# Kernel optimization log

Measured on AMD Instinct MI355X. Metric: run time of the kernel, lower is better.

The kernel has to match this reference:

```python
import jax, jax.numpy as jnp
import numpy as np

DIM = 384
RES = 32
NH = 8
RD = 2
B = 64


def _linear_params(key, out_f, in_f, scale=0.02, bias=True):
    kw, kb = jax.random.split(key)
    W = jax.random.normal(kw, (out_f, in_f), dtype=jnp.float32) * scale
    b = jax.random.normal(kb, (out_f,), dtype=jnp.float32) * scale if bias else None
    return W, b


def setup_inputs() -> dict:
    key = jax.random.key(0)
    ks = jax.random.split(key, 16)
    x = jax.random.normal(ks[0], (B, RES, RES, DIM), dtype=jnp.float32)
    Wc_h, bc_h = _linear_params(ks[1], NH * RD, DIM)
    Wg_h, bg_h = _linear_params(ks[2], RES * RES, RES * RD)
    Wo_h, bo_h = _linear_params(ks[3], DIM, DIM)
    Wc_w, bc_w = _linear_params(ks[4], NH * RD, DIM)
    Wg_w, bg_w = _linear_params(ks[5], RES * RES, RES * RD)
    Wo_w, bo_w = _linear_params(ks[6], DIM, DIM)
    Wmlpc, _ = _linear_params(ks[7], DIM, DIM, bias=False)
    Wr1, br1 = _linear_params(ks[8], DIM // 4, DIM)
    Wr2, br2 = _linear_params(ks[9], DIM * 3, DIM // 4)
    Wp, bp = _linear_params(ks[10], DIM, DIM)
    return dict(x=x, Wc_h=Wc_h, bc_h=bc_h, Wg_h=Wg_h, bg_h=bg_h, Wo_h=Wo_h, bo_h=bo_h,
                Wc_w=Wc_w, bc_w=bc_w, Wg_w=Wg_w, bg_w=bg_w, Wo_w=Wo_w, bo_w=bo_w,
                Wmlpc=Wmlpc, Wr1=Wr1, br1=br1, Wr2=Wr2, br2=br2, Wp=Wp, bp=bp)


def _dynamixer_op(x, Wc, bc, Wg, bg, Wo, bo):
    # x: [N, L, C]
    N, L, C = x.shape
    hd = C // NH
    # compress -> [N, L, NH*RD] -> [N, NH, L*RD]
    w = x @ Wc.T + bc
    w = w.reshape(N, L, NH, RD).transpose(0, 2, 1, 3).reshape(N, NH, L * RD)
    # generate -> [N, NH, L, L], softmax over axis -2 (rows)
    w = (w @ Wg.T + bg).reshape(N, NH, L, L)
    w = jax.nn.softmax(w, axis=-2)
    # x -> [N, NH, hd, L]; mix: y[n,h,d,j] = sum_l x[n,h,d,l] * w[n,h,l,j]
    xh = x.reshape(N, L, NH, hd).transpose(0, 2, 3, 1)
    y = jnp.einsum('nhdl,nhlj->nhdj', xh, w)
    y = y.transpose(0, 3, 1, 2).reshape(N, L, C)
    return y @ Wo.T + bo


def reference(x, Wc_h, bc_h, Wg_h, bg_h, Wo_h, bo_h,
              Wc_w, bc_w, Wg_w, bg_w, Wo_w, bo_w,
              Wmlpc, Wr1, br1, Wr2, br2, Wp, bp):
    Bn, H, W, C = x.shape
    # mix along H: batch over (B, W)
    h = _dynamixer_op(x.transpose(0, 2, 1, 3).reshape(Bn * W, H, C),
                      Wc_h, bc_h, Wg_h, bg_h, Wo_h, bo_h)
    h = h.reshape(Bn, W, H, C).transpose(0, 2, 1, 3)
    # mix along W: batch over (B, H)
    w = _dynamixer_op(x.reshape(Bn * H, W, C),
                      Wc_w, bc_w, Wg_w, bg_w, Wo_w, bo_w)
    w = w.reshape(Bn, H, W, C)
    # channel path (no bias)
    c = x @ Wmlpc.T
    # reweighting: global average pool over H, W
    a = (h + w + c).mean(axis=(1, 2))            # [B, C]
    a = jax.nn.gelu(a @ Wr1.T + br1, approximate=False) @ Wr2.T + br2  # [B, 3C]
    a = a.reshape(Bn, C, 3).transpose(2, 0, 1)   # [3, B, C]
    a = jax.nn.softmax(a, axis=0)[:, :, None, None, :]  # [3, B, 1, 1, C]
    out = h * a[0] + w * a[1] + c * a[2]
    return out @ Wp.T + bp
```

## Files before the change

kernel.cpp:

```cpp
#include <hip/hip_runtime.h>

typedef unsigned short u16;
typedef __bf16 bf16_t;
typedef bf16_t bf16x8 __attribute__((ext_vector_type(8)));
typedef float f32x4 __attribute__((ext_vector_type(4)));

__device__ __forceinline__ u16 f2b(float f) {
  union { float f; unsigned u; } v; v.f = f;
  unsigned r = (v.u + 0x7fffu + ((v.u >> 16) & 1u)) >> 16;
  return (u16)r;
}
__device__ __forceinline__ float b2f(u16 b) {
  union { unsigned u; float f; } v; v.u = ((unsigned)b) << 16;
  return v.f;
}
__device__ __forceinline__ f32x4 mfma16(bf16x8 a, bf16x8 b, f32x4 c) {
  return __builtin_amdgcn_mfma_f32_16x16x32_bf16(a, b, c, 0, 0, 0);
}

struct CvtJobs {
  const float* s[8];
  u16* d[8];
  int n[8];
};
__global__ void k0_cvt(CvtJobs j) {
  int job = blockIdx.y;
  const float* s = j.s[job];
  u16* d = j.d[job];
  int n = j.n[job];
  int stride = gridDim.x * blockDim.x * 4;
  for (int i = (blockIdx.x * blockDim.x + threadIdx.x) * 4; i < n; i += stride) {
    float4 v = *(const float4*)(s + i);
    ushort4 o4;
    o4.x = f2b(v.x); o4.y = f2b(v.y); o4.z = f2b(v.z); o4.w = f2b(v.w);
    *(ushort4*)(d + i) = o4;
  }
}

#define LW 392
#define TW 40
#define AW 40

__global__ __launch_bounds__(256, 2) void k1_mixer(
    const float* __restrict__ x,
    const u16* __restrict__ Wc_h_b, const float* __restrict__ bc_h,
    const u16* __restrict__ Wg_h_b, const float* __restrict__ bg_h,
    const u16* __restrict__ Wc_w_b, const float* __restrict__ bc_w,
    const u16* __restrict__ Wg_w_b, const float* __restrict__ bg_w,
    u16* __restrict__ y_h, u16* y_w,
    float* __restrict__ psum_yh, float* __restrict__ psum_yw,
    float* __restrict__ psum_x)
{
  __shared__ u16 xs_b[32 * LW];
  __shared__ u16 xs_t[384 * TW];
  __shared__ u16 attn[8 * 32 * AW];
  __shared__ u16 whead[16 * 72];

  const int tid = threadIdx.x;
  const int bid = blockIdx.x;
  const int path = bid >> 11;
  const int n = bid & 2047;
  const int b = n >> 5, o = n & 31;
  long base; int strideL;
  if (path == 0) { base = (long)b * 393216 + (long)o * 384;   strideL = 12288; }
  else           { base = (long)b * 393216 + (long)o * 12288; strideL = 384; }
  const float* xseq = x + base;

  const u16* Wc_b = path ? Wc_w_b : Wc_h_b;
  const float* bc = path ? bc_w : bc_h;
  const u16* Wg_b = path ? Wg_w_b : Wg_h_b;
  const float* bg = path ? bg_w : bg_h;

  for (int i = tid; i < 3072; i += 256) {
    int l = i / 96, c4 = (i % 96) * 4;
    float4 v = *(const float4*)(xseq + (long)l * strideL + c4);
    ushort4 w4;
    w4.x = f2b(v.x); w4.y = f2b(v.y); w4.z = f2b(v.z); w4.w = f2b(v.w);
    *(ushort4*)&xs_b[l * LW + c4] = w4;
  }
  for (int i = tid; i < 576; i += 256) whead[576 + i] = 0;
  __syncthreads();

  for (int i = tid; i < 3072; i += 256) {
    int c = i % 384, l4 = (i / 384) * 4;
    ushort4 w4;
    w4.x = xs_b[(l4 + 0) * LW + c];
    w4.y = xs_b[(l4 + 1) * LW + c];
    w4.z = xs_b[(l4 + 2) * LW + c];
    w4.w = xs_b[(l4 + 3) * LW + c];
    *(ushort4*)&xs_t[c * TW + l4] = w4;
  }
  if (path == 0) {
    for (int c = tid; c < 384; c += 256) {
      float s = 0.f;
      for (int l = 0; l < 32; l++) s += b2f(xs_b[l * LW + c]);
      psum_x[(long)n * 384 + c] = s;
    }
  }

  const int wave = tid >> 6, lane = tid & 63;
  const int lq = lane >> 4, lr = lane & 15;
  const f32x4 z = {0.f, 0.f, 0.f, 0.f};

  if (wave < 2) {
    f32x4 acc = z;
    for (int ks = 0; ks < 12; ks++) {
      bf16x8 af  = *(const bf16x8*)&xs_b[(wave * 16 + lr) * LW + ks * 32 + lq * 8];
      bf16x8 bfr = *(const bf16x8*)(Wc_b + lr * 384 + ks * 32 + lq * 8);
      acc = mfma16(af, bfr, acc);
    }
    float bcv = bc[lr];
    for (int r = 0; r < 4; r++) {
      int l = wave * 16 + lq * 4 + r;
      whead[(lr >> 1) * 72 + l * 2 + (lr & 1)] = f2b(acc[r] + bcv);
    }
  }
  __syncthreads();

  {
    bf16x8 ga0 = *(const bf16x8*)&whead[lr * 72 + lq * 8];
    bf16x8 ga1 = *(const bf16x8*)&whead[lr * 72 + 32 + lq * 8];
    for (int t = 0; t < 16; t++) {
      int nt = wave * 16 + t;
      const u16* wg = Wg_b + (nt * 16 + lr) * 64;
      bf16x8 gb0 = *(const bf16x8*)(wg + lq * 8);
      bf16x8 gb1 = *(const bf16x8*)(wg + 32 + lq * 8);
      f32x4 acc = z;
      acc = mfma16(ga0, gb0, acc);
      acc = mfma16(ga1, gb1, acc);
      if (lq < 2) {
        int m = nt * 16 + lr, ii = m >> 5, jj = m & 31;
        for (int r = 0; r < 4; r++)
          attn[((lq * 4 + r) * 32 + jj) * AW + ii] = f2b(acc[r]);
      }
    }
  }
  __syncthreads();

  {
    int h = tid >> 5, j = tid & 31;
    u16* row = &attn[(h * 32 + j) * AW];
    float v[32]; float mx = -1e30f;
    for (int i = 0; i < 32; i++) {
      v[i] = b2f(row[i]) + bg[i * 32 + j];
      mx = fmaxf(mx, v[i]);
    }
    float s = 0.f;
    for (int i = 0; i < 32; i++) { v[i] = __expf(v[i] - mx); s += v[i]; }
    float inv = 1.0f / s;
    for (int i = 0; i < 32; i++) row[i] = f2b(v[i] * inv);
  }
  __syncthreads();

  for (int hh = 0; hh < 2; hh++) {
    int h = wave * 2 + hh;
    bf16x8 bf0 = *(const bf16x8*)&attn[(h * 32 + lr) * AW + lq * 8];
    bf16x8 bf1 = *(const bf16x8*)&attn[(h * 32 + 16 + lr) * AW + lq * 8];
    for (int mt = 0; mt < 3; mt++) {
      bf16x8 af = *(const bf16x8*)&xs_t[(h * 48 + mt * 16 + lr) * TW + lq * 8];
      f32x4 a0 = mfma16(af, bf0, z);
      f32x4 a1 = mfma16(af, bf1, z);
      for (int r = 0; r < 4; r++) {
        int c = h * 48 + mt * 16 + lq * 4 + r;
        xs_b[lr * LW + c]        = f2b(a0[r]);
        xs_b[(16 + lr) * LW + c] = f2b(a1[r]);
      }
    }
  }
  __syncthreads();

  if (path == 0) {
    u16* yout = y_h + base;
    for (int i = tid; i < 1536; i += 256) {
      int l = i / 48, uu = (i % 48) * 8;
      *(uint4*)(yout + (long)l * 12288 + uu) = *(const uint4*)&xs_b[l * LW + uu];
    }
  } else {
    u16* yout = y_w + (long)(n * 32) * 768;
    for (int i = tid; i < 1536; i += 256) {
      int l = i / 48, uu = (i % 48) * 8;
      *(uint4*)(yout + (long)l * 768 + uu) = *(const uint4*)&xs_b[l * LW + uu];
    }
  }
  {
    float* pdst = (path ? psum_yw : psum_yh) + (long)n * 384;
    for (int c = tid; c < 384; c += 256) {
      float s = 0.f;
      for (int jj = 0; jj < 32; jj++) s += b2f(xs_b[jj * LW + c]);
      pdst[c] = s;
    }
  }
}

__global__ __launch_bounds__(384) void k3_scales(
    const float* __restrict__ psum_yh, const float* __restrict__ psum_yw,
    const float* __restrict__ psum_x,
    const float* __restrict__ Wo_h, const float* __restrict__ bo_h,
    const float* __restrict__ Wo_w, const float* __restrict__ bo_w,
    const float* __restrict__ Wmlpc,
    const float* __restrict__ Wr1, const float* __restrict__ br1,
    const float* __restrict__ Wr2, const float* __restrict__ br2,
    float* __restrict__ scal)
{
  __shared__ float ph[384], pw[384], px[384], a[384], r1[96];
  int b = blockIdx.x, t = threadIdx.x;
  float sh = 0.f, sw = 0.f, sx = 0.f;
  for (int o = 0; o < 32; o++) {
    sh += psum_yh[(long)(b * 32 + o) * 384 + t];
    sw += psum_yw[(long)(b * 32 + o) * 384 + t];
    sx += psum_x[(long)(b * 32 + o) * 384 + t];
  }
  ph[t] = sh; pw[t] = sw; px[t] = sx;
  __syncthreads();
  float s1 = 0.f, s2 = 0.f, s3 = 0.f;
  for (int k = 0; k < 384; k++) {
    s1 += ph[k] * Wo_h[t * 384 + k];
    s2 += pw[k] * Wo_w[t * 384 + k];
    s3 += px[k] * Wmlpc[t * 384 + k];
  }
  a[t] = (s1 + s2 + s3) * (1.f / 1024.f) + bo_h[t] + bo_w[t];
  __syncthreads();
  if (t < 96) {
    float s = 0.f;
    for (int k = 0; k < 384; k++) s += a[k] * Wr1[t * 384 + k];
    s += br1[t];
    r1[t] = s * 0.5f * (1.f + erff(s * 0.70710678118654752f));
  }
  __syncthreads();
  {
    float sv[3];
    for (int si = 0; si < 3; si++) {
      float acc = 0.f;
      for (int k = 0; k < 96; k++) acc += r1[k] * Wr2[(t * 3 + si) * 96 + k];
      sv[si] = acc + br2[t * 3 + si];
    }
    float mx = fmaxf(sv[0], fmaxf(sv[1], sv[2]));
    float e0 = __expf(sv[0] - mx), e1 = __expf(sv[1] - mx), e2 = __expf(sv[2] - mx);
    float inv = 1.f / (e0 + e1 + e2);
    scal[0 * 24576 + b * 384 + t] = e0 * inv;
    scal[1 * 24576 + b * 384 + t] = e1 * inv;
    scal[2 * 24576 + b * 384 + t] = e2 * inv;
  }
}

__device__ __forceinline__ void gemm_regB(
    const u16* __restrict__ Bglob, const u16* __restrict__ bufA,
    f32x4 acc[4][3], int wn, int lq, int lr)
{
  const u16* bp0 = Bglob + (wn * 48 + lr) * 384 + lq * 8;
  const u16* ap0 = bufA + lr * 392 + lq * 8;
  bf16x8 bcur[3], af[4];
#pragma unroll
  for (int nt = 0; nt < 3; nt++) bcur[nt] = *(const bf16x8*)(bp0 + nt * 6144);
#pragma unroll
  for (int mt = 0; mt < 4; mt++) af[mt] = *(const bf16x8*)(ap0 + mt * 6272);
  for (int ks = 0; ks < 12; ks++) {
    bf16x8 bnx[3], an[4];
    const int k1 = (ks < 11 ? ks + 1 : 11) * 32;
#pragma unroll
    for (int nt = 0; nt < 3; nt++) bnx[nt] = *(const bf16x8*)(bp0 + nt * 6144 + k1);
#pragma unroll
    for (int mt = 0; mt < 4; mt++) an[mt] = *(const bf16x8*)(ap0 + mt * 6272 + k1);
#pragma unroll
    for (int nt = 0; nt < 3; nt++)
#pragma unroll
      for (int mt = 0; mt < 4; mt++)
        acc[mt][nt] = mfma16(af[mt], bcur[nt], acc[mt][nt]);
#pragma unroll
    for (int nt = 0; nt < 3; nt++) bcur[nt] = bnx[nt];
#pragma unroll
    for (int mt = 0; mt < 4; mt++) af[mt] = an[mt];
  }
}

__global__ __launch_bounds__(512, 6) void k24_final(
    const float* __restrict__ x, const u16* __restrict__ y_h, const u16* y_w,
    const u16* __restrict__ Wo_h_b, const u16* __restrict__ Wo_w_b,
    const u16* __restrict__ Wmlpc_b, const u16* __restrict__ Wp_b,
    const float* __restrict__ bo_h, const float* __restrict__ bo_w,
    const float* __restrict__ bp,
    const float* __restrict__ scal, float* out)
{
  __shared__ u16 bufA[64 * 392];

  const int tid = threadIdx.x;
  const int m0 = blockIdx.x * 64;
  const int b = m0 >> 10;
  const int wave = tid >> 6, lane = tid & 63;
  const int lq = lane >> 4, lr = lane & 15;
  const int wn = wave;
  const f32x4 z = {0.f, 0.f, 0.f, 0.f};

  for (int i = tid; i < 6144; i += 512) {
    int row = i / 96, c4 = (i % 96) * 4;
    float4 v = *(const float4*)(x + (long)(m0 + row) * 384 + c4);
    ushort4 w4;
    w4.x = f2b(v.x); w4.y = f2b(v.y); w4.z = f2b(v.z); w4.w = f2b(v.w);
    *(ushort4*)&bufA[row * 392 + c4] = w4;
  }
  __syncthreads();

  f32x4 acc[4][3];
#pragma unroll
  for (int i = 0; i < 4; i++)
#pragma unroll
    for (int jn = 0; jn < 3; jn++) acc[i][jn] = z;

  gemm_regB(Wmlpc_b, bufA, acc, wn, lq, lr);
  {
    const float* s2p = scal + 2 * 24576 + b * 384;
    const float* s1p = scal + 1 * 24576 + b * 384;
#pragma unroll
    for (int nt = 0; nt < 3; nt++) {
      int col = wn * 48 + nt * 16 + lr;
      float r = s2p[col] / fmaxf(s1p[col], 1e-30f);
#pragma unroll
      for (int mt = 0; mt < 4; mt++)
#pragma unroll
        for (int rr = 0; rr < 4; rr++) acc[mt][nt][rr] *= r;
    }
  }
  __syncthreads();

  for (int i = tid; i < 3072; i += 512) {
    int row = i / 48, u8 = (i % 48) * 8;
    *(uint4*)&bufA[row * 392 + u8] = *(const uint4*)(y_w + (long)(m0 + row) * 768 + u8);
  }
  __syncthreads();

  gemm_regB(Wo_w_b, bufA, acc, wn, lq, lr);
  {
    const float* s1p = scal + 1 * 24576 + b * 384;
    const float* s0p = scal + 0 * 24576 + b * 384;
#pragma unroll
    for (int nt = 0; nt < 3; nt++) {
      int col = wn * 48 + nt * 16 + lr;
      float r = s1p[col] / fmaxf(s0p[col], 1e-30f);
#pragma unroll
      for (int mt = 0; mt < 4; mt++)
#pragma unroll
        for (int rr = 0; rr < 4; rr++) acc[mt][nt][rr] *= r;
    }
  }
  __syncthreads();

  for (int i = tid; i < 3072; i += 512) {
    int row = i / 48, u8 = (i % 48) * 8;
    *(uint4*)&bufA[row * 392 + u8] = *(const uint4*)(y_h + (long)(m0 + row) * 384 + u8);
  }
  __syncthreads();

  gemm_regB(Wo_h_b, bufA, acc, wn, lq, lr);
  __syncthreads();

  {
    const float* s0p = scal + 0 * 24576 + b * 384;
    const float* s1p = scal + 1 * 24576 + b * 384;
#pragma unroll
    for (int nt = 0; nt < 3; nt++) {
      int col = wn * 48 + nt * 16 + lr;
      float s0v = s0p[col];
      float bcb = s0v * bo_h[col] + s1p[col] * bo_w[col];
#pragma unroll
      for (int mt = 0; mt < 4; mt++)
#pragma unroll
        for (int r = 0; r < 4; r++) {
          int row = mt * 16 + lq * 4 + r;
          bufA[row * 392 + col] = f2b(acc[mt][nt][r] * s0v + bcb);
        }
    }
  }
  __syncthreads();

#pragma unroll
  for (int i = 0; i < 4; i++)
#pragma unroll
    for (int jn = 0; jn < 3; jn++) acc[i][jn] = z;
  gemm_regB(Wp_b, bufA, acc, wn, lq, lr);
#pragma unroll
  for (int nt = 0; nt < 3; nt++) {
    int col = wn * 48 + nt * 16 + lr;
    float bi = bp[col];
#pragma unroll
    for (int mt = 0; mt < 4; mt++)
#pragma unroll
      for (int r = 0; r < 4; r++) {
        int row = m0 + mt * 16 + lq * 4 + r;
        out[(long)row * 384 + col] = acc[mt][nt][r] + bi;
      }
  }
}

extern "C" void kernel_launch(void* const* d_in, const int* in_sizes, int n_in,
                              void* d_out, int out_size, void* d_ws, size_t ws_size,
                              hipStream_t stream) {
  const float* x     = (const float*)d_in[0];
  const float* Wc_h  = (const float*)d_in[1];
  const float* bc_h  = (const float*)d_in[2];
  const float* Wg_h  = (const float*)d_in[3];
  const float* bg_h  = (const float*)d_in[4];
  const float* Wo_h  = (const float*)d_in[5];
  const float* bo_h  = (const float*)d_in[6];
  const float* Wc_w  = (const float*)d_in[7];
  const float* bc_w  = (const float*)d_in[8];
  const float* Wg_w  = (const float*)d_in[9];
  const float* bg_w  = (const float*)d_in[10];
  const float* Wo_w  = (const float*)d_in[11];
  const float* bo_w  = (const float*)d_in[12];
  const float* Wmlpc = (const float*)d_in[13];
  const float* Wr1   = (const float*)d_in[14];
  const float* br1   = (const float*)d_in[15];
  const float* Wr2   = (const float*)d_in[16];
  const float* br2   = (const float*)d_in[17];
  const float* Wp    = (const float*)d_in[18];
  const float* bp    = (const float*)d_in[19];
  float* out = (float*)d_out;

  char* ws = (char*)d_ws;
  u16* y_h       = (u16*)(ws + 0);
  float* psum_yh = (float*)(ws + 50331648);
  float* psum_yw = (float*)(ws + 53477376);
  float* psum_x  = (float*)(ws + 56623104);
  float* scal    = (float*)(ws + 59768832);
  u16* Wc_h_b    = (u16*)(ws + 60063744);
  u16* Wc_w_b    = (u16*)(ws + 60076032);
  u16* Wg_h_b    = (u16*)(ws + 60088320);
  u16* Wg_w_b    = (u16*)(ws + 60219392);
  u16* Wo_h_b    = (u16*)(ws + 60350464);
  u16* Wo_w_b    = (u16*)(ws + 60645376);
  u16* Wmlpc_b   = (u16*)(ws + 60940288);
  u16* Wp_b      = (u16*)(ws + 61235200);

  u16* y_w = (u16*)d_out;

  CvtJobs jobs;
  jobs.s[0] = Wc_h;  jobs.d[0] = Wc_h_b;  jobs.n[0] = 6144;
  jobs.s[1] = Wc_w;  jobs.d[1] = Wc_w_b;  jobs.n[1] = 6144;
  jobs.s[2] = Wg_h;  jobs.d[2] = Wg_h_b;  jobs.n[2] = 65536;
  jobs.s[3] = Wg_w;  jobs.d[3] = Wg_w_b;  jobs.n[3] = 65536;
  jobs.s[4] = Wo_h;  jobs.d[4] = Wo_h_b;  jobs.n[4] = 147456;
  jobs.s[5] = Wo_w;  jobs.d[5] = Wo_w_b;  jobs.n[5] = 147456;
  jobs.s[6] = Wmlpc; jobs.d[6] = Wmlpc_b; jobs.n[6] = 147456;
  jobs.s[7] = Wp;    jobs.d[7] = Wp_b;    jobs.n[7] = 147456;
  k0_cvt<<<dim3(144, 8), 256, 0, stream>>>(jobs);

  k1_mixer<<<4096, 256, 0, stream>>>(x, Wc_h_b, bc_h, Wg_h_b, bg_h,
      Wc_w_b, bc_w, Wg_w_b, bg_w, y_h, y_w, psum_yh, psum_yw, psum_x);

  k3_scales<<<64, 384, 0, stream>>>(psum_yh, psum_yw, psum_x, Wo_h, bo_h,
      Wo_w, bo_w, Wmlpc, Wr1, br1, Wr2, br2, scal);

  k24_final<<<1024, 512, 0, stream>>>(x, y_h, y_w,
      Wo_h_b, Wo_w_b, Wmlpc_b, Wp_b, bo_h, bo_w, bp, scal, out);
}
```

Baseline: 703.5 us.

## Pack y_h/y_w into one interleaved buffer and retile final GEMM waves 2x4

The two mixer outputs are now written into one buffer in the output allocation. Each row holds the H-path result in its first half and the W-path result in its second half, so the separate y_h workspace region is gone and the final kernel reads both from adjacent memory. The final fused GEMM kernel changes its wave layout from 8 waves spanning columns (4x3 MFMA tiles each) to a 2x4 grid (2x6 tiles each). This halves the A fragments each wave reads from LDS but doubles the weight fragments each wave loads from global memory, with the two row-waves fetching the same B columns.

After: 853.0 us. 21.3% more time.

```diff
diff --git a/kernel.cpp b/kernel.cpp
--- a/kernel.cpp
+++ b/kernel.cpp
@@ -47,7 +47,7 @@
     const u16* __restrict__ Wg_h_b, const float* __restrict__ bg_h,
     const u16* __restrict__ Wc_w_b, const float* __restrict__ bc_w,
     const u16* __restrict__ Wg_w_b, const float* __restrict__ bg_w,
-    u16* __restrict__ y_h, u16* y_w,
+    u16* ypack,
     float* __restrict__ psum_yh, float* __restrict__ psum_yw,
     float* __restrict__ psum_x)
 {
@@ -170,13 +170,13 @@
   __syncthreads();
 
   if (path == 0) {
-    u16* yout = y_h + base;
+    u16* yout = ypack + ((long)b * 1024 + o) * 768;
     for (int i = tid; i < 1536; i += 256) {
       int l = i / 48, uu = (i % 48) * 8;
-      *(uint4*)(yout + (long)l * 12288 + uu) = *(const uint4*)&xs_b[l * LW + uu];
+      *(uint4*)(yout + (long)l * 24576 + uu) = *(const uint4*)&xs_b[l * LW + uu];
     }
   } else {
-    u16* yout = y_w + (long)(n * 32) * 768;
+    u16* yout = ypack + (long)(n * 32) * 768 + 384;
     for (int i = tid; i < 1536; i += 256) {
       int l = i / 48, uu = (i % 48) * 8;
       *(uint4*)(yout + (long)l * 768 + uu) = *(const uint4*)&xs_b[l * LW + uu];
@@ -245,36 +245,36 @@
 
 __device__ __forceinline__ void gemm_regB(
     const u16* __restrict__ Bglob, const u16* __restrict__ bufA,
-    f32x4 acc[4][3], int wn, int lq, int lr)
+    f32x4 acc[2][6], int wm, int wn, int lq, int lr)
 {
-  const u16* bp0 = Bglob + (wn * 48 + lr) * 384 + lq * 8;
-  const u16* ap0 = bufA + lr * 392 + lq * 8;
-  bf16x8 bcur[3], af[4];
-#pragma unroll
-  for (int nt = 0; nt < 3; nt++) bcur[nt] = *(const bf16x8*)(bp0 + nt * 6144);
-#pragma unroll
-  for (int mt = 0; mt < 4; mt++) af[mt] = *(const bf16x8*)(ap0 + mt * 6272);
+  const u16* bp0 = Bglob + (wn * 96 + lr) * 384 + lq * 8;
+  const u16* ap0 = bufA + (wm * 32 + lr) * 392 + lq * 8;
+  bf16x8 bcur[6], af[2];
+#pragma unroll
+  for (int nt = 0; nt < 6; nt++) bcur[nt] = *(const bf16x8*)(bp0 + nt * 6144);
+#pragma unroll
+  for (int mt = 0; mt < 2; mt++) af[mt] = *(const bf16x8*)(ap0 + mt * 6272);
   for (int ks = 0; ks < 12; ks++) {
-    bf16x8 bnx[3], an[4];
+    bf16x8 bnx[6], an[2];
     const int k1 = (ks < 11 ? ks + 1 : 11) * 32;
 #pragma unroll
-    for (int nt = 0; nt < 3; nt++) bnx[nt] = *(const bf16x8*)(bp0 + nt * 6144 + k1);
-#pragma unroll
-    for (int mt = 0; mt < 4; mt++) an[mt] = *(const bf16x8*)(ap0 + mt * 6272 + k1);
-#pragma unroll
-    for (int nt = 0; nt < 3; nt++)
-#pragma unroll
-      for (int mt = 0; mt < 4; mt++)
+    for (int nt = 0; nt < 6; nt++) bnx[nt] = *(const bf16x8*)(bp0 + nt * 6144 + k1);
+#pragma unroll
+    for (int mt = 0; mt < 2; mt++) an[mt] = *(const bf16x8*)(ap0 + mt * 6272 + k1);
+#pragma unroll
+    for (int nt = 0; nt < 6; nt++)
+#pragma unroll
+      for (int mt = 0; mt < 2; mt++)
         acc[mt][nt] = mfma16(af[mt], bcur[nt], acc[mt][nt]);
 #pragma unroll
-    for (int nt = 0; nt < 3; nt++) bcur[nt] = bnx[nt];
-#pragma unroll
-    for (int mt = 0; mt < 4; mt++) af[mt] = an[mt];
+    for (int nt = 0; nt < 6; nt++) bcur[nt] = bnx[nt];
+#pragma unroll
+    for (int mt = 0; mt < 2; mt++) af[mt] = an[mt];
   }
 }
 
 __global__ __launch_bounds__(512, 6) void k24_final(
-    const float* __restrict__ x, const u16* __restrict__ y_h, const u16* y_w,
+    const float* __restrict__ x, const u16* ypack,
     const u16* __restrict__ Wo_h_b, const u16* __restrict__ Wo_w_b,
     const u16* __restrict__ Wmlpc_b, const u16* __restrict__ Wp_b,
     const float* __restrict__ bo_h, const float* __restrict__ bo_w,
@@ -288,7 +288,7 @@
   const int b = m0 >> 10;
   const int wave = tid >> 6, lane = tid & 63;
   const int lq = lane >> 4, lr = lane & 15;
-  const int wn = wave;
+  const int wm = wave >> 2, wn = wave & 3;
   const f32x4 z = {0.f, 0.f, 0.f, 0.f};
 
   for (int i = tid; i < 6144; i += 512) {
@@ -300,22 +300,22 @@
   }
   __syncthreads();
 
-  f32x4 acc[4][3];
-#pragma unroll
-  for (int i = 0; i < 4; i++)
-#pragma unroll
-    for (int jn = 0; jn < 3; jn++) acc[i][jn] = z;
-
-  gemm_regB(Wmlpc_b, bufA, acc, wn, lq, lr);
+  f32x4 acc[2][6];
+#pragma unroll
+  for (int i = 0; i < 2; i++)
+#pragma unroll
+    for (int jn = 0; jn < 6; jn++) acc[i][jn] = z;
+
+  gemm_regB(Wmlpc_b, bufA, acc, wm, wn, lq, lr);
   {
     const float* s2p = scal + 2 * 24576 + b * 384;
     const float* s1p = scal + 1 * 24576 + b * 384;
 #pragma unroll
-    for (int nt = 0; nt < 3; nt++) {
-      int col = wn * 48 + nt * 16 + lr;
+    for (int nt = 0; nt < 6; nt++) {
+      int col = wn * 96 + nt * 16 + lr;
       float r = s2p[col] / fmaxf(s1p[col], 1e-30f);
 #pragma unroll
-      for (int mt = 0; mt < 4; mt++)
+      for (int mt = 0; mt < 2; mt++)
 #pragma unroll
         for (int rr = 0; rr < 4; rr++) acc[mt][nt][rr] *= r;
     }
@@ -324,20 +324,21 @@
 
   for (int i = tid; i < 3072; i += 512) {
     int row = i / 48, u8 = (i % 48) * 8;
-    *(uint4*)&bufA[row * 392 + u8] = *(const uint4*)(y_w + (long)(m0 + row) * 768 + u8);
-  }
-  __syncthreads();
-
-  gemm_regB(Wo_w_b, bufA, acc, wn, lq, lr);
+    *(uint4*)&bufA[row * 392 + u8] =
+        *(const uint4*)(ypack + (long)(m0 + row) * 768 + 384 + u8);
+  }
+  __syncthreads();
+
+  gemm_regB(Wo_w_b, bufA, acc, wm, wn, lq, lr);
   {
     const float* s1p = scal + 1 * 24576 + b * 384;
     const float* s0p = scal + 0 * 24576 + b * 384;
 #pragma unroll
-    for (int nt = 0; nt < 3; nt++) {
-      int col = wn * 48 + nt * 16 + lr;
+    for (int nt = 0; nt < 6; nt++) {
+      int col = wn * 96 + nt * 16 + lr;
       float r = s1p[col] / fmaxf(s0p[col], 1e-30f);
 #pragma unroll
-      for (int mt = 0; mt < 4; mt++)
+      for (int mt = 0; mt < 2; mt++)
 #pragma unroll
         for (int rr = 0; rr < 4; rr++) acc[mt][nt][rr] *= r;
     }
@@ -346,26 +347,27 @@
 
   for (int i = tid; i < 3072; i += 512) {
     int row = i / 48, u8 = (i % 48) * 8;
-    *(uint4*)&bufA[row * 392 + u8] = *(const uint4*)(y_h + (long)(m0 + row) * 384 + u8);
-  }
-  __syncthreads();
-
-  gemm_regB(Wo_h_b, bufA, acc, wn, lq, lr);
+    *(uint4*)&bufA[row * 392 + u8] =
+        *(const uint4*)(ypack + (long)(m0 + row) * 768 + u8);
+  }
+  __syncthreads();
+
+  gemm_regB(Wo_h_b, bufA, acc, wm, wn, lq, lr);
   __syncthreads();
 
   {
     const float* s0p = scal + 0 * 24576 + b * 384;
     const float* s1p = scal + 1 * 24576 + b * 384;
 #pragma unroll
-    for (int nt = 0; nt < 3; nt++) {
-      int col = wn * 48 + nt * 16 + lr;
+    for (int nt = 0; nt < 6; nt++) {
+      int col = wn * 96 + nt * 16 + lr;
       float s0v = s0p[col];
       float bcb = s0v * bo_h[col] + s1p[col] * bo_w[col];
 #pragma unroll
-      for (int mt = 0; mt < 4; mt++)
+      for (int mt = 0; mt < 2; mt++)
 #pragma unroll
         for (int r = 0; r < 4; r++) {
-          int row = mt * 16 + lq * 4 + r;
+          int row = wm * 32 + mt * 16 + lq * 4 + r;
           bufA[row * 392 + col] = f2b(acc[mt][nt][r] * s0v + bcb);
         }
     }
@@ -373,19 +375,19 @@
   __syncthreads();
 
 #pragma unroll
-  for (int i = 0; i < 4; i++)
-#pragma unroll
-    for (int jn = 0; jn < 3; jn++) acc[i][jn] = z;
-  gemm_regB(Wp_b, bufA, acc, wn, lq, lr);
-#pragma unroll
-  for (int nt = 0; nt < 3; nt++) {
-    int col = wn * 48 + nt * 16 + lr;
+  for (int i = 0; i < 2; i++)
+#pragma unroll
+    for (int jn = 0; jn < 6; jn++) acc[i][jn] = z;
+  gemm_regB(Wp_b, bufA, acc, wm, wn, lq, lr);
+#pragma unroll
+  for (int nt = 0; nt < 6; nt++) {
+    int col = wn * 96 + nt * 16 + lr;
     float bi = bp[col];
 #pragma unroll
-    for (int mt = 0; mt < 4; mt++)
+    for (int mt = 0; mt < 2; mt++)
 #pragma unroll
       for (int r = 0; r < 4; r++) {
-        int row = m0 + mt * 16 + lq * 4 + r;
+        int row = m0 + wm * 32 + mt * 16 + lq * 4 + r;
         out[(long)row * 384 + col] = acc[mt][nt][r] + bi;
       }
   }
@@ -417,7 +419,6 @@
   float* out = (float*)d_out;
 
   char* ws = (char*)d_ws;
-  u16* y_h       = (u16*)(ws + 0);
   float* psum_yh = (float*)(ws + 50331648);
   float* psum_yw = (float*)(ws + 53477376);
   float* psum_x  = (float*)(ws + 56623104);
@@ -431,7 +432,7 @@
   u16* Wmlpc_b   = (u16*)(ws + 60940288);
   u16* Wp_b      = (u16*)(ws + 61235200);
 
-  u16* y_w = (u16*)d_out;
+  u16* ypack = (u16*)d_out;
 
   CvtJobs jobs;
   jobs.s[0] = Wc_h;  jobs.d[0] = Wc_h_b;  jobs.n[0] = 6144;
@@ -445,11 +446,11 @@
   k0_cvt<<<dim3(144, 8), 256, 0, stream>>>(jobs);
 
   k1_mixer<<<4096, 256, 0, stream>>>(x, Wc_h_b, bc_h, Wg_h_b, bg_h,
-      Wc_w_b, bc_w, Wg_w_b, bg_w, y_h, y_w, psum_yh, psum_yw, psum_x);
+      Wc_w_b, bc_w, Wg_w_b, bg_w, ypack, psum_yh, psum_yw, psum_x);
 
   k3_scales<<<64, 384, 0, stream>>>(psum_yh, psum_yw, psum_x, Wo_h, bo_h,
       Wo_w, bo_w, Wmlpc, Wr1, br1, Wr2, br2, scal);
 
-  k24_final<<<1024, 512, 0, stream>>>(x, y_h, y_w,
+  k24_final<<<1024, 512, 0, stream>>>(x, ypack,
       Wo_h_b, Wo_w_b, Wmlpc_b, Wp_b, bo_h, bo_w, bp, scal, out);
 }
```
